# Performance work log

Hardware: AMD Instinct MI355X
Metric: run time of the kernel (lower is better)

## Reference

```python
import jax, jax.numpy as jnp
import numpy as np

N = 100000   # nodes
E = 500000   # edges
DN = 64      # node feat dim
DE = 64      # edge feat dim
D = 128      # hidden = in_feats = out_feats
TD = 64      # time-encoding dim


def setup_inputs() -> dict:
    key = jax.random.key(0)
    ks = jax.random.split(key, 20)
    s = 0.05
    inp = {
        'nfeat': jax.random.normal(ks[0], (N, DN), dtype=jnp.float32),
        'efeat': jax.random.normal(ks[1], (E, DE), dtype=jnp.float32),
        'src': jax.random.randint(ks[2], (E,), 0, N),
        'dst': jax.random.randint(ks[3], (E,), 0, N),
        'ts': jax.random.uniform(ks[4], (E,), dtype=jnp.float32) * 1000.0,
    }
    i = 5
    for l in (1, 2):
        inp[f'W_self{l}'] = jax.random.normal(ks[i], (D + TD, D), dtype=jnp.float32) * s; i += 1
        inp[f'b_self{l}'] = jnp.zeros((D,), dtype=jnp.float32)
        inp[f'W_neigh{l}'] = jax.random.normal(ks[i], (D, D), dtype=jnp.float32) * s; i += 1
        inp[f'b_neigh{l}'] = jnp.zeros((D,), dtype=jnp.float32)
        inp[f'omega{l}'] = jax.random.normal(ks[i], (TD,), dtype=jnp.float32); i += 1
        inp[f'phase{l}'] = jax.random.normal(ks[i], (TD,), dtype=jnp.float32); i += 1
    return inp


def _tsage_layer(src_prev, dst_prev, src, dst, ts, W_self, b_self, W_neigh, b_neigh, omega, phase):
    # cosine time encoding per edge: [E, TD]
    te = jnp.cos(ts[:, None] * omega[None, :] + phase[None, :])
    # temporal-neighborhood mean: per node, mean of features of incident edges
    sum_n = (jax.ops.segment_sum(dst_prev, src, num_segments=N)
             + jax.ops.segment_sum(src_prev, dst, num_segments=N))      # [N, D]
    ones = jnp.ones((src.shape[0], 1), dtype=src_prev.dtype)
    cnt = (jax.ops.segment_sum(ones, src, num_segments=N)
           + jax.ops.segment_sum(ones, dst, num_segments=N))            # [N, 1]
    mean_n = sum_n / jnp.maximum(cnt, 1.0)                              # [N, D]
    neigh_proj = mean_n @ W_neigh + b_neigh                             # project once per node
    src_out = jnp.concatenate([src_prev, te], axis=1) @ W_self + b_self + neigh_proj[src]
    dst_out = jnp.concatenate([dst_prev, te], axis=1) @ W_self + b_self + neigh_proj[dst]
    # dropout in eval mode (identity), then activation (relu)
    return jax.nn.relu(src_out), jax.nn.relu(dst_out)


def reference(nfeat, efeat, src, dst, ts,
              W_self1, b_self1, W_neigh1, b_neigh1, omega1, phase1,
              W_self2, b_self2, W_neigh2, b_neigh2, omega2, phase2):
    # combine_feats: per-edge gather-concat of endpoint node feats with edge feats
    src_feat = jnp.concatenate([nfeat[src], efeat], axis=1)  # [E, D]
    dst_feat = jnp.concatenate([nfeat[dst], efeat], axis=1)  # [E, D]
    params = [
        (W_self1, b_self1, W_neigh1, b_neigh1, omega1, phase1),
        (W_self2, b_self2, W_neigh2, b_neigh2, omega2, phase2),
    ]
    for p in params:
        src_feat, dst_feat = _tsage_layer(src_feat, dst_feat, src, dst, ts, *p)
    return src_feat, dst_feat
```

## Files before the change

kernel.cpp:

```cpp
#include <hip/hip_runtime.h>
#include <cstdint>
#include <cmath>

#define NN 100000
#define EE 500000
#define CAP 48

typedef __attribute__((ext_vector_type(8))) short short8v;
typedef __attribute__((ext_vector_type(4))) float f32x4;

static __device__ __forceinline__ unsigned short f2bf_rne(float x) {
    unsigned u = __float_as_uint(x);
    u += 0x7FFFu + ((u >> 16) & 1u);
    return (unsigned short)(u >> 16);
}

static __device__ __forceinline__ void split8(float4 a, float4 b,
                                              short8v* hi, short8v* lo) {
    union { short8v v; unsigned u[4]; } H, L;
    float f[8] = {a.x, a.y, a.z, a.w, b.x, b.y, b.z, b.w};
#pragma unroll
    for (int p = 0; p < 4; ++p) {
        unsigned u0 = __float_as_uint(f[2 * p]);
        unsigned u1 = __float_as_uint(f[2 * p + 1]);
        H.u[p] = (u0 >> 16) | (u1 & 0xFFFF0000u);
        float r0 = f[2 * p]     - __uint_as_float(u0 & 0xFFFF0000u);
        float r1 = f[2 * p + 1] - __uint_as_float(u1 & 0xFFFF0000u);
        L.u[p] = (unsigned)f2bf_rne(r0) | ((unsigned)f2bf_rne(r1) << 16);
    }
    *hi = H.v; *lo = L.v;
}

static __device__ __forceinline__ void lds_dma16(const void* g, void* l) {
    __builtin_amdgcn_global_load_lds(
        (const __attribute__((address_space(1))) unsigned int*)g,
        (__attribute__((address_space(3))) unsigned int*)l, 16, 0, 0);
}

__global__ __launch_bounds__(256) void k_build(const int* __restrict__ src,
                                               const int* __restrict__ dst,
                                               int* __restrict__ pos,
                                               int2* __restrict__ inc) {
    int e = blockIdx.x * 256 + threadIdx.x;
    if (e >= EE) return;
    int s = src[e], d = dst[e];
    int sl = atomicAdd(&pos[s], 1);
    if (sl < CAP) inc[(size_t)s * CAP + sl] = make_int2((e << 1) | 1, d);
    int dl = atomicAdd(&pos[d], 1);
    if (dl < CAP) inc[(size_t)d * CAP + dl] = make_int2((e << 1), s);
}

__global__ __launch_bounds__(256) void k_wt(const float* __restrict__ W, int K,
                                            unsigned short* __restrict__ H,
                                            unsigned short* __restrict__ L) {
    int idx = blockIdx.x * 256 + threadIdx.x;
    if (idx >= K * 128) return;
    int k = idx >> 7, c = idx & 127;
    float x = W[idx];
    unsigned u = __float_as_uint(x);
    H[(size_t)c * K + k] = (unsigned short)(u >> 16);
    float r = x - __uint_as_float(u & 0xFFFF0000u);
    L[(size_t)c * K + k] = f2bf_rne(r);
}

template <int LAYER>
__global__ __launch_bounds__(256) void k_agg(const float* __restrict__ featS,
                                             const float* __restrict__ featD,
                                             const float* __restrict__ nfeat,
                                             const float* __restrict__ efeat,
                                             const int* __restrict__ pos,
                                             const int2* __restrict__ inc,
                                             float* __restrict__ mean) {
    int w = (blockIdx.x * 256 + threadIdx.x) >> 6;
    int lane = threadIdx.x & 63;
    if (w >= NN) return;
    int q = lane >> 4, cl = lane & 15;
    int d = pos[w];
    int dd = min(d, CAP);
    const int2* lst = inc + (size_t)w * CAP;
    float a0 = 0.f, a1 = 0.f, a2 = 0.f, a3 = 0.f;
    float a4 = 0.f, a5 = 0.f, a6 = 0.f, a7 = 0.f;
    for (int j = q; j < dd; j += 4) {
        int2 en = lst[j];
        int e = en.x >> 1, side = en.x & 1;
        const float* p;
        if (LAYER == 1) {
            p = (cl < 8) ? (nfeat + (size_t)en.y * 64 + cl * 8)
                         : (efeat + (size_t)e * 64 + (cl - 8) * 8);
        } else {
            p = (side ? featD : featS) + (size_t)e * 128 + cl * 8;
        }
        float4 v0 = *(const float4*)p;
        float4 v1 = *(const float4*)(p + 4);
        a0 += v0.x; a1 += v0.y; a2 += v0.z; a3 += v0.w;
        a4 += v1.x; a5 += v1.y; a6 += v1.z; a7 += v1.w;
    }
#pragma unroll
    for (int m = 16; m <= 32; m <<= 1) {
        a0 += __shfl_xor(a0, m); a1 += __shfl_xor(a1, m);
        a2 += __shfl_xor(a2, m); a3 += __shfl_xor(a3, m);
        a4 += __shfl_xor(a4, m); a5 += __shfl_xor(a5, m);
        a6 += __shfl_xor(a6, m); a7 += __shfl_xor(a7, m);
    }
    if (q == 0) {
        float inv = 1.0f / fmaxf((float)d, 1.0f);
        float4 r0, r1;
        r0.x = a0 * inv; r0.y = a1 * inv; r0.z = a2 * inv; r0.w = a3 * inv;
        r1.x = a4 * inv; r1.y = a5 * inv; r1.z = a6 * inv; r1.w = a7 * inv;
        *(float4*)(mean + (size_t)w * 128 + cl * 8) = r0;
        *(float4*)(mean + (size_t)w * 128 + cl * 8 + 4) = r1;
    }
}

__global__ __launch_bounds__(256) void k_neigh_mfma(
        const float* __restrict__ mean,
        const unsigned short* __restrict__ WtH,
        const unsigned short* __restrict__ WtL,
        const float* __restrict__ bias,
        float* __restrict__ outp) {
    const int tid  = threadIdx.x;
    const int n0   = blockIdx.x * 128;
    const int lane = tid & 63;
    const int w    = tid >> 6;
    const int wr   = w >> 1, wc = w & 1;
    const int krow = lane & 15;
    const int kgrp = lane >> 4;

    const float* rb[4];
#pragma unroll
    for (int rt = 0; rt < 4; ++rt) {
        int n = min(n0 + wr * 64 + rt * 16 + krow, NN - 1);
        rb[rt] = mean + (size_t)n * 128;
    }

    f32x4 acc[4][4] = {};
#pragma unroll
    for (int ch = 0; ch < 4; ++ch) {
        const int koff = ch * 32 + kgrp * 8;
        short8v Ah[4], Al[4];
#pragma unroll
        for (int rt = 0; rt < 4; ++rt) {
            float4 x0 = *(const float4*)(rb[rt] + koff);
            float4 x1 = *(const float4*)(rb[rt] + koff + 4);
            split8(x0, x1, &Ah[rt], &Al[rt]);
        }
        short8v Bh[4], Bl[4];
#pragma unroll
        for (int ct = 0; ct < 4; ++ct) {
            int c = wc * 64 + ct * 16 + krow;
            Bh[ct] = *(const short8v*)(WtH + (size_t)c * 128 + koff);
            Bl[ct] = *(const short8v*)(WtL + (size_t)c * 128 + koff);
        }
#pragma unroll
        for (int ct = 0; ct < 4; ++ct)
#pragma unroll
            for (int rt = 0; rt < 4; ++rt) {
                acc[rt][ct] = __builtin_amdgcn_mfma_f32_16x16x32_bf16(Ah[rt], Bh[ct], acc[rt][ct], 0, 0, 0);
                acc[rt][ct] = __builtin_amdgcn_mfma_f32_16x16x32_bf16(Ah[rt], Bl[ct], acc[rt][ct], 0, 0, 0);
                acc[rt][ct] = __builtin_amdgcn_mfma_f32_16x16x32_bf16(Al[rt], Bh[ct], acc[rt][ct], 0, 0, 0);
            }
    }

    float bcol[4];
#pragma unroll
    for (int ct = 0; ct < 4; ++ct) bcol[ct] = bias[wc * 64 + ct * 16 + krow];
#pragma unroll
    for (int rt = 0; rt < 4; ++rt)
#pragma unroll
        for (int j = 0; j < 4; ++j) {
            int n = n0 + wr * 64 + rt * 16 + kgrp * 4 + j;
            if (n < NN) {
                float* op = outp + (size_t)n * 128;
#pragma unroll
                for (int ct = 0; ct < 4; ++ct)
                    op[wc * 64 + ct * 16 + krow] = acc[rt][ct][j] + bcol[ct];
            }
        }
}

template <int LAYER>
__global__ __launch_bounds__(256) void k_edge_mfma(
        const float* __restrict__ featS, const float* __restrict__ featD,
        const float* __restrict__ nfeat, const float* __restrict__ efeat,
        float* __restrict__ outS, float* __restrict__ outD,
        const int* __restrict__ src, const int* __restrict__ dst,
        const float* __restrict__ ts,
        const unsigned short* __restrict__ WtH,
        const unsigned short* __restrict__ WtL,
        const float* __restrict__ bias,
        const float* __restrict__ neigh,
        const float* __restrict__ omega, const float* __restrict__ phase) {
    __shared__ float Abuf[2][128][32];
    __shared__ unsigned short teH[64][72];
    __shared__ unsigned short teL[64][72];

    const int tid  = threadIdx.x;
    const int e0   = blockIdx.x * 64;
    const int lane = tid & 63;
    const int w    = tid >> 6;
    const int wr   = w >> 1, wc = w & 1;
    const int krow = lane & 15;
    const int kgrp = lane >> 4;

    {
        const int tl = tid & 63;
        const int j0 = (tid >> 6) * 16;
        const float tval = ts[min(e0 + tl, EE - 1)];
#pragma unroll
        for (int j = 0; j < 16; j += 2) {
            int jj = j0 + j;
            float c0 = cosf(fmaf(tval, omega[jj],     phase[jj]));
            float c1 = cosf(fmaf(tval, omega[jj + 1], phase[jj + 1]));
            unsigned u0 = __float_as_uint(c0), u1 = __float_as_uint(c1);
            *(unsigned*)&teH[tl][jj] = (u0 >> 16) | (u1 & 0xFFFF0000u);
            float r0 = c0 - __uint_as_float(u0 & 0xFFFF0000u);
            float r1 = c1 - __uint_as_float(u1 & 0xFFFF0000u);
            *(unsigned*)&teL[tl][jj] =
                (unsigned)f2bf_rne(r0) | ((unsigned)f2bf_rne(r1) << 16);
        }
    }

    const float* gbN[4];
    const float* gbE[4];
#pragma unroll
    for (int qq = 0; qq < 4; ++qq) {
        int row = w * 32 + qq * 8 + (lane >> 3);
        int e = min(e0 + (row & 63), EE - 1);
        if (LAYER == 1) {
            int node = (row < 64) ? src[e] : dst[e];
            gbN[qq] = nfeat + (size_t)node * 64;
            gbE[qq] = efeat + (size_t)e * 64;
        } else {
            gbN[qq] = ((row < 64) ? featS : featD) + (size_t)e * 128;
            gbE[qq] = nullptr;
        }
    }
    const int pslot = lane & 7;

    auto dma_chunk = [&](int b, int ch) {
#pragma unroll
        for (int qq = 0; qq < 4; ++qq) {
            int row = w * 32 + qq * 8 + (lane >> 3);
            int pg = (pslot - row) & 7;
            const float* gsrc;
            if (LAYER == 1)
                gsrc = ((ch < 2) ? (gbN[qq] + ch * 32) : (gbE[qq] + (ch - 2) * 32)) + pg * 4;
            else
                gsrc = gbN[qq] + ch * 32 + pg * 4;
            lds_dma16(gsrc, &Abuf[b][(w * 4 + qq) * 8][0]);
        }
    };

    f32x4 acc[4][4] = {};
    dma_chunk(0, 0);

#pragma unroll
    for (int ch = 0; ch < 4; ++ch) {
        __syncthreads();
        if (ch < 3) dma_chunk((ch + 1) & 1, ch + 1);
        const int b = ch & 1;
        const int koff = ch * 32 + kgrp * 8;
        short8v Ah[4], Al[4];
#pragma unroll
        for (int rt = 0; rt < 4; ++rt) {
            int row = wr * 64 + rt * 16 + krow;
            float4 x0 = *(const float4*)&Abuf[b][row][(((2 * kgrp)     + row) & 7) * 4];
            float4 x1 = *(const float4*)&Abuf[b][row][(((2 * kgrp + 1) + row) & 7) * 4];
            split8(x0, x1, &Ah[rt], &Al[rt]);
        }
        short8v Bh[4], Bl[4];
#pragma unroll
        for (int ct = 0; ct < 4; ++ct) {
            int c = wc * 64 + ct * 16 + krow;
            Bh[ct] = *(const short8v*)(WtH + (size_t)c * 192 + koff);
            Bl[ct] = *(const short8v*)(WtL + (size_t)c * 192 + koff);
        }
#pragma unroll
        for (int ct = 0; ct < 4; ++ct)
#pragma unroll
            for (int rt = 0; rt < 4; ++rt) {
                acc[rt][ct] = __builtin_amdgcn_mfma_f32_16x16x32_bf16(Ah[rt], Bh[ct], acc[rt][ct], 0, 0, 0);
                acc[rt][ct] = __builtin_amdgcn_mfma_f32_16x16x32_bf16(Ah[rt], Bl[ct], acc[rt][ct], 0, 0, 0);
                acc[rt][ct] = __builtin_amdgcn_mfma_f32_16x16x32_bf16(Al[rt], Bh[ct], acc[rt][ct], 0, 0, 0);
            }
    }

#pragma unroll
    for (int ch = 4; ch < 6; ++ch) {
        const int koff = ch * 32 + kgrp * 8;
        const int kt = koff - 128;
        short8v Ah[4], Al[4];
#pragma unroll
        for (int rt = 0; rt < 4; ++rt) {
            int el = rt * 16 + krow;
            Ah[rt] = *(const short8v*)&teH[el][kt];
            Al[rt] = *(const short8v*)&teL[el][kt];
        }
        short8v Bh[4], Bl[4];
#pragma unroll
        for (int ct = 0; ct < 4; ++ct) {
            int c = wc * 64 + ct * 16 + krow;
            Bh[ct] = *(const short8v*)(WtH + (size_t)c * 192 + koff);
            Bl[ct] = *(const short8v*)(WtL + (size_t)c * 192 + koff);
        }
#pragma unroll
        for (int ct = 0; ct < 4; ++ct)
#pragma unroll
            for (int rt = 0; rt < 4; ++rt) {
                acc[rt][ct] = __builtin_amdgcn_mfma_f32_16x16x32_bf16(Ah[rt], Bh[ct], acc[rt][ct], 0, 0, 0);
                acc[rt][ct] = __builtin_amdgcn_mfma_f32_16x16x32_bf16(Ah[rt], Bl[ct], acc[rt][ct], 0, 0, 0);
                acc[rt][ct] = __builtin_amdgcn_mfma_f32_16x16x32_bf16(Al[rt], Bh[ct], acc[rt][ct], 0, 0, 0);
            }
    }

    float bcol[4];
#pragma unroll
    for (int ct = 0; ct < 4; ++ct) bcol[ct] = bias[wc * 64 + ct * 16 + krow];
#pragma unroll
    for (int rt = 0; rt < 4; ++rt)
#pragma unroll
        for (int j = 0; j < 4; ++j) {
            int row = wr * 64 + rt * 16 + kgrp * 4 + j;
            int e = e0 + (row & 63);
            if (e < EE) {
                bool isS = row < 64;
                int node = isS ? src[e] : dst[e];
                const float* np = neigh + (size_t)node * 128;
                float* op = (isS ? outS : outD) + (size_t)e * 128;
#pragma unroll
                for (int ct = 0; ct < 4; ++ct) {
                    int col = wc * 64 + ct * 16 + krow;
                    float v2 = acc[rt][ct][j] + bcol[ct] + np[col];
                    op[col] = fmaxf(v2, 0.f);
                }
            }
        }
}

extern "C" void kernel_launch(void* const* d_in, const int* in_sizes, int n_in,
                              void* d_out, int out_size, void* d_ws, size_t ws_size,
                              hipStream_t stream) {
    const float* nfeat = (const float*)d_in[0];
    const float* efeat = (const float*)d_in[1];
    const int*   src   = (const int*)d_in[2];
    const int*   dst   = (const int*)d_in[3];
    const float* ts    = (const float*)d_in[4];
    const float* Wself[2]  = {(const float*)d_in[5],  (const float*)d_in[11]};
    const float* bself[2]  = {(const float*)d_in[6],  (const float*)d_in[12]};
    const float* Wneigh[2] = {(const float*)d_in[7],  (const float*)d_in[13]};
    const float* bneigh[2] = {(const float*)d_in[8],  (const float*)d_in[14]};
    const float* omega[2]  = {(const float*)d_in[9],  (const float*)d_in[15]};
    const float* phase[2]  = {(const float*)d_in[10], (const float*)d_in[16]};

    float* outS = (float*)d_out;
    float* outD = outS + (size_t)EE * 128;

    float* mean  = (float*)d_ws;
    float* neigh = mean + (size_t)NN * 128;
    int*   pos   = (int*)(neigh + (size_t)NN * 128);
    int2*  inc   = (int2*)(pos + NN);
    unsigned short* wb = (unsigned short*)(inc + (size_t)NN * CAP);
    unsigned short* WsH[2] = {wb,                 wb + 2 * 128 * 192};
    unsigned short* WsL[2] = {wb + 128 * 192,     wb + 3 * 128 * 192};
    unsigned short* wn = wb + 4 * 128 * 192;
    unsigned short* WnH[2] = {wn,                 wn + 2 * 128 * 128};
    unsigned short* WnL[2] = {wn + 128 * 128,     wn + 3 * 128 * 128};

    hipMemsetAsync(pos, 0, NN * sizeof(int), stream);
    k_build<<<(EE + 255) / 256, 256, 0, stream>>>(src, dst, pos, inc);
    for (int l = 0; l < 2; ++l) {
        k_wt<<<(192 * 128 + 255) / 256, 256, 0, stream>>>(Wself[l], 192, WsH[l], WsL[l]);
        k_wt<<<(128 * 128 + 255) / 256, 256, 0, stream>>>(Wneigh[l], 128, WnH[l], WnL[l]);
    }

    k_agg<1><<<(NN * 64 + 255) / 256, 256, 0, stream>>>(outS, outD, nfeat, efeat,
                                                        pos, inc, mean);
    k_neigh_mfma<<<(NN + 127) / 128, 256, 0, stream>>>(mean, WnH[0], WnL[0], bneigh[0], neigh);
    k_edge_mfma<1><<<(EE + 63) / 64, 256, 0, stream>>>(outS, outD, nfeat, efeat,
                                                       outS, outD, src, dst, ts,
                                                       WsH[0], WsL[0], bself[0], neigh,
                                                       omega[0], phase[0]);

    k_agg<2><<<(NN * 64 + 255) / 256, 256, 0, stream>>>(outS, outD, nfeat, efeat,
                                                        pos, inc, mean);
    k_neigh_mfma<<<(NN + 127) / 128, 256, 0, stream>>>(mean, WnH[1], WnL[1], bneigh[1], neigh);
    k_edge_mfma<2><<<(EE + 63) / 64, 256, 0, stream>>>(outS, outD, nfeat, efeat,
                                                       outS, outD, src, dst, ts,
                                                       WsH[1], WsL[1], bself[1], neigh,
                                                       omega[1], phase[1]);
}
```

Baseline: 1.913 ms.

## Fuse neighbor projection into edge GEMM by concatenating mean rows along K

Removes the separate per-node neighbor-projection kernel. Each edge row now gathers its endpoint's mean vector as four extra K-chunks and multiplies against a combined 320-row weight (W_self stacked with W_neigh), with both biases added in the epilogue. The A-tile staging moves from double to triple buffering with explicit vmcnt waits, and the aggregation loop prefetches the next incidence entry. This drops the neigh buffer round trip and its gather in the epilogue, but it redoes the 128x128 projection per edge endpoint (about 10x more MFMA work for that part) and gathers 512 B mean rows per edge row.

```diff
diff --git a/kernel.cpp b/kernel.cpp
--- a/kernel.cpp
+++ b/kernel.cpp
@@ -50,17 +50,18 @@
     if (dl < CAP) inc[(size_t)d * CAP + dl] = make_int2((e << 1), s);
 }
 
-__global__ __launch_bounds__(256) void k_wt(const float* __restrict__ W, int K,
-                                            unsigned short* __restrict__ H,
-                                            unsigned short* __restrict__ L) {
+__global__ __launch_bounds__(256) void k_wt2(const float* __restrict__ Wself,
+                                             const float* __restrict__ Wneigh,
+                                             unsigned short* __restrict__ H,
+                                             unsigned short* __restrict__ L) {
     int idx = blockIdx.x * 256 + threadIdx.x;
-    if (idx >= K * 128) return;
+    if (idx >= 320 * 128) return;
     int k = idx >> 7, c = idx & 127;
-    float x = W[idx];
+    float x = (k < 192) ? Wself[k * 128 + c] : Wneigh[(k - 192) * 128 + c];
     unsigned u = __float_as_uint(x);
-    H[(size_t)c * K + k] = (unsigned short)(u >> 16);
+    H[(size_t)c * 320 + k] = (unsigned short)(u >> 16);
     float r = x - __uint_as_float(u & 0xFFFF0000u);
-    L[(size_t)c * K + k] = f2bf_rne(r);
+    L[(size_t)c * 320 + k] = f2bf_rne(r);
 }
 
 template <int LAYER>
@@ -80,8 +81,9 @@
     const int2* lst = inc + (size_t)w * CAP;
     float a0 = 0.f, a1 = 0.f, a2 = 0.f, a3 = 0.f;
     float a4 = 0.f, a5 = 0.f, a6 = 0.f, a7 = 0.f;
+    int2 en = (q < dd) ? lst[q] : make_int2(0, 0);
     for (int j = q; j < dd; j += 4) {
-        int2 en = lst[j];
+        int2 nxt = (j + 4 < dd) ? lst[j + 4] : en;
         int e = en.x >> 1, side = en.x & 1;
         const float* p;
         if (LAYER == 1) {
@@ -94,6 +96,7 @@
         float4 v1 = *(const float4*)(p + 4);
         a0 += v0.x; a1 += v0.y; a2 += v0.z; a3 += v0.w;
         a4 += v1.x; a5 += v1.y; a6 += v1.z; a7 += v1.w;
+        en = nxt;
     }
 #pragma unroll
     for (int m = 16; m <= 32; m <<= 1) {
@@ -112,85 +115,19 @@
     }
 }
 
-__global__ __launch_bounds__(256) void k_neigh_mfma(
-        const float* __restrict__ mean,
-        const unsigned short* __restrict__ WtH,
-        const unsigned short* __restrict__ WtL,
-        const float* __restrict__ bias,
-        float* __restrict__ outp) {
-    const int tid  = threadIdx.x;
-    const int n0   = blockIdx.x * 128;
-    const int lane = tid & 63;
-    const int w    = tid >> 6;
-    const int wr   = w >> 1, wc = w & 1;
-    const int krow = lane & 15;
-    const int kgrp = lane >> 4;
-
-    const float* rb[4];
-#pragma unroll
-    for (int rt = 0; rt < 4; ++rt) {
-        int n = min(n0 + wr * 64 + rt * 16 + krow, NN - 1);
-        rb[rt] = mean + (size_t)n * 128;
-    }
-
-    f32x4 acc[4][4] = {};
-#pragma unroll
-    for (int ch = 0; ch < 4; ++ch) {
-        const int koff = ch * 32 + kgrp * 8;
-        short8v Ah[4], Al[4];
-#pragma unroll
-        for (int rt = 0; rt < 4; ++rt) {
-            float4 x0 = *(const float4*)(rb[rt] + koff);
-            float4 x1 = *(const float4*)(rb[rt] + koff + 4);
-            split8(x0, x1, &Ah[rt], &Al[rt]);
-        }
-        short8v Bh[4], Bl[4];
-#pragma unroll
-        for (int ct = 0; ct < 4; ++ct) {
-            int c = wc * 64 + ct * 16 + krow;
-            Bh[ct] = *(const short8v*)(WtH + (size_t)c * 128 + koff);
-            Bl[ct] = *(const short8v*)(WtL + (size_t)c * 128 + koff);
-        }
-#pragma unroll
-        for (int ct = 0; ct < 4; ++ct)
-#pragma unroll
-            for (int rt = 0; rt < 4; ++rt) {
-                acc[rt][ct] = __builtin_amdgcn_mfma_f32_16x16x32_bf16(Ah[rt], Bh[ct], acc[rt][ct], 0, 0, 0);
-                acc[rt][ct] = __builtin_amdgcn_mfma_f32_16x16x32_bf16(Ah[rt], Bl[ct], acc[rt][ct], 0, 0, 0);
-                acc[rt][ct] = __builtin_amdgcn_mfma_f32_16x16x32_bf16(Al[rt], Bh[ct], acc[rt][ct], 0, 0, 0);
-            }
-    }
-
-    float bcol[4];
-#pragma unroll
-    for (int ct = 0; ct < 4; ++ct) bcol[ct] = bias[wc * 64 + ct * 16 + krow];
-#pragma unroll
-    for (int rt = 0; rt < 4; ++rt)
-#pragma unroll
-        for (int j = 0; j < 4; ++j) {
-            int n = n0 + wr * 64 + rt * 16 + kgrp * 4 + j;
-            if (n < NN) {
-                float* op = outp + (size_t)n * 128;
-#pragma unroll
-                for (int ct = 0; ct < 4; ++ct)
-                    op[wc * 64 + ct * 16 + krow] = acc[rt][ct][j] + bcol[ct];
-            }
-        }
-}
-
 template <int LAYER>
-__global__ __launch_bounds__(256) void k_edge_mfma(
+__global__ __launch_bounds__(256) void k_edge_fused(
         const float* __restrict__ featS, const float* __restrict__ featD,
         const float* __restrict__ nfeat, const float* __restrict__ efeat,
+        const float* __restrict__ mean,
         float* __restrict__ outS, float* __restrict__ outD,
         const int* __restrict__ src, const int* __restrict__ dst,
         const float* __restrict__ ts,
         const unsigned short* __restrict__ WtH,
         const unsigned short* __restrict__ WtL,
-        const float* __restrict__ bias,
-        const float* __restrict__ neigh,
+        const float* __restrict__ bs, const float* __restrict__ bn,
         const float* __restrict__ omega, const float* __restrict__ phase) {
-    __shared__ float Abuf[2][128][32];
+    __shared__ float Abuf[3][128][32];
     __shared__ unsigned short teH[64][72];
     __shared__ unsigned short teL[64][72];
 
@@ -219,48 +156,77 @@
                 (unsigned)f2bf_rne(r0) | ((unsigned)f2bf_rne(r1) << 16);
         }
     }
-
-    const float* gbN[4];
+    asm volatile("s_waitcnt lgkmcnt(0)" ::: "memory");
+    __builtin_amdgcn_sched_barrier(0);
+
+    int nodeq[4];
+    const float* gbF[4];
     const float* gbE[4];
 #pragma unroll
     for (int qq = 0; qq < 4; ++qq) {
         int row = w * 32 + qq * 8 + (lane >> 3);
         int e = min(e0 + (row & 63), EE - 1);
+        int node = (row < 64) ? src[e] : dst[e];
+        nodeq[qq] = node;
         if (LAYER == 1) {
-            int node = (row < 64) ? src[e] : dst[e];
-            gbN[qq] = nfeat + (size_t)node * 64;
+            gbF[qq] = nfeat + (size_t)node * 64;
             gbE[qq] = efeat + (size_t)e * 64;
         } else {
-            gbN[qq] = ((row < 64) ? featS : featD) + (size_t)e * 128;
+            gbF[qq] = ((row < 64) ? featS : featD) + (size_t)e * 128;
             gbE[qq] = nullptr;
         }
     }
     const int pslot = lane & 7;
 
-    auto dma_chunk = [&](int b, int ch) {
+    auto dma = [&](int j) {
 #pragma unroll
         for (int qq = 0; qq < 4; ++qq) {
             int row = w * 32 + qq * 8 + (lane >> 3);
             int pg = (pslot - row) & 7;
             const float* gsrc;
-            if (LAYER == 1)
-                gsrc = ((ch < 2) ? (gbN[qq] + ch * 32) : (gbE[qq] + (ch - 2) * 32)) + pg * 4;
-            else
-                gsrc = gbN[qq] + ch * 32 + pg * 4;
-            lds_dma16(gsrc, &Abuf[b][(w * 4 + qq) * 8][0]);
+            if (j < 4) {
+                if (LAYER == 1)
+                    gsrc = (j < 2) ? (gbF[qq] + j * 32 + pg * 4)
+                                   : (gbE[qq] + (j - 2) * 32 + pg * 4);
+                else
+                    gsrc = gbF[qq] + j * 32 + pg * 4;
+            } else {
+                gsrc = mean + (size_t)nodeq[qq] * 128 + (j - 4) * 32 + pg * 4;
+            }
+            lds_dma16(gsrc, &Abuf[j % 3][(w * 4 + qq) * 8][0]);
         }
     };
 
     f32x4 acc[4][4] = {};
-    dma_chunk(0, 0);
-
-#pragma unroll
-    for (int ch = 0; ch < 4; ++ch) {
-        __syncthreads();
-        if (ch < 3) dma_chunk((ch + 1) & 1, ch + 1);
-        const int b = ch & 1;
-        const int koff = ch * 32 + kgrp * 8;
+
+    dma(0);
+    dma(1);
+    asm volatile("s_waitcnt vmcnt(4)" ::: "memory");
+    __builtin_amdgcn_sched_barrier(0);
+
+#pragma unroll
+    for (int j = 0; j < 8; ++j) {
+        const int kb = (j < 4) ? j * 32 : 192 + (j - 4) * 32;
+        __builtin_amdgcn_s_barrier();
+        __builtin_amdgcn_sched_barrier(0);
+
+        const int koff = kb + kgrp * 8;
+        short8v Bh[4], Bl[4];
+#pragma unroll
+        for (int ct = 0; ct < 4; ++ct) {
+            int c = wc * 64 + ct * 16 + krow;
+            Bh[ct] = *(const short8v*)(WtH + (size_t)c * 320 + koff);
+            Bl[ct] = *(const short8v*)(WtL + (size_t)c * 320 + koff);
+        }
+        __builtin_amdgcn_sched_barrier(0);
+        if (j < 6) dma(j + 2);
+        __builtin_amdgcn_sched_barrier(0);
+        if (j < 7) { asm volatile("s_waitcnt vmcnt(4)" ::: "memory"); }
+        else       { asm volatile("s_waitcnt vmcnt(0)" ::: "memory"); }
+        __builtin_amdgcn_sched_barrier(0);
+
         short8v Ah[4], Al[4];
+        const int b = j % 3;
 #pragma unroll
         for (int rt = 0; rt < 4; ++rt) {
             int row = wr * 64 + rt * 16 + krow;
@@ -268,13 +234,6 @@
             float4 x1 = *(const float4*)&Abuf[b][row][(((2 * kgrp + 1) + row) & 7) * 4];
             split8(x0, x1, &Ah[rt], &Al[rt]);
         }
-        short8v Bh[4], Bl[4];
-#pragma unroll
-        for (int ct = 0; ct < 4; ++ct) {
-            int c = wc * 64 + ct * 16 + krow;
-            Bh[ct] = *(const short8v*)(WtH + (size_t)c * 192 + koff);
-            Bl[ct] = *(const short8v*)(WtL + (size_t)c * 192 + koff);
-        }
 #pragma unroll
         for (int ct = 0; ct < 4; ++ct)
 #pragma unroll
@@ -286,22 +245,23 @@
     }
 
 #pragma unroll
-    for (int ch = 4; ch < 6; ++ch) {
-        const int koff = ch * 32 + kgrp * 8;
-        const int kt = koff - 128;
+    for (int tc = 0; tc < 2; ++tc) {
+        const int kb = 128 + tc * 32;
+        const int koff = kb + kgrp * 8;
+        const int kt = tc * 32 + kgrp * 8;
+        short8v Bh[4], Bl[4];
+#pragma unroll
+        for (int ct = 0; ct < 4; ++ct) {
+            int c = wc * 64 + ct * 16 + krow;
+            Bh[ct] = *(const short8v*)(WtH + (size_t)c * 320 + koff);
+            Bl[ct] = *(const short8v*)(WtL + (size_t)c * 320 + koff);
+        }
         short8v Ah[4], Al[4];
 #pragma unroll
         for (int rt = 0; rt < 4; ++rt) {
             int el = rt * 16 + krow;
             Ah[rt] = *(const short8v*)&teH[el][kt];
             Al[rt] = *(const short8v*)&teL[el][kt];
-        }
-        short8v Bh[4], Bl[4];
-#pragma unroll
-        for (int ct = 0; ct < 4; ++ct) {
-            int c = wc * 64 + ct * 16 + krow;
-            Bh[ct] = *(const short8v*)(WtH + (size_t)c * 192 + koff);
-            Bl[ct] = *(const short8v*)(WtL + (size_t)c * 192 + koff);
         }
 #pragma unroll
         for (int ct = 0; ct < 4; ++ct)
@@ -315,23 +275,22 @@
 
     float bcol[4];
 #pragma unroll
-    for (int ct = 0; ct < 4; ++ct) bcol[ct] = bias[wc * 64 + ct * 16 + krow];
+    for (int ct = 0; ct < 4; ++ct) {
+        int col = wc * 64 + ct * 16 + krow;
+        bcol[ct] = bs[col] + bn[col];
+    }
 #pragma unroll
     for (int rt = 0; rt < 4; ++rt)
 #pragma unroll
-        for (int j = 0; j < 4; ++j) {
-            int row = wr * 64 + rt * 16 + kgrp * 4 + j;
+        for (int jj = 0; jj < 4; ++jj) {
+            int row = wr * 64 + rt * 16 + kgrp * 4 + jj;
             int e = e0 + (row & 63);
             if (e < EE) {
-                bool isS = row < 64;
-                int node = isS ? src[e] : dst[e];
-                const float* np = neigh + (size_t)node * 128;
-                float* op = (isS ? outS : outD) + (size_t)e * 128;
+                float* op = ((row < 64) ? outS : outD) + (size_t)e * 128;
 #pragma unroll
                 for (int ct = 0; ct < 4; ++ct) {
                     int col = wc * 64 + ct * 16 + krow;
-                    float v2 = acc[rt][ct][j] + bcol[ct] + np[col];
-                    op[col] = fmaxf(v2, 0.f);
+                    op[col] = fmaxf(acc[rt][ct][jj] + bcol[ct], 0.f);
                 }
             }
         }
@@ -355,37 +314,29 @@
     float* outS = (float*)d_out;
     float* outD = outS + (size_t)EE * 128;
 
-    float* mean  = (float*)d_ws;
-    float* neigh = mean + (size_t)NN * 128;
-    int*   pos   = (int*)(neigh + (size_t)NN * 128);
-    int2*  inc   = (int2*)(pos + NN);
+    float* mean = (float*)d_ws;
+    int*   pos  = (int*)(mean + (size_t)NN * 128);
+    int2*  inc  = (int2*)(pos + NN);
     unsigned short* wb = (unsigned short*)(inc + (size_t)NN * CAP);
-    unsigned short* WsH[2] = {wb,                 wb + 2 * 128 * 192};
-    unsigned short* WsL[2] = {wb + 128 * 192,     wb + 3 * 128 * 192};
-    unsigned short* wn = wb + 4 * 128 * 192;
-    unsigned short* WnH[2] = {wn,                 wn + 2 * 128 * 128};
-    unsigned short* WnL[2] = {wn + 128 * 128,     wn + 3 * 128 * 128};
+    unsigned short* WH[2] = {wb,                 wb + 2 * 320 * 128};
+    unsigned short* WL[2] = {wb + 320 * 128,     wb + 3 * 320 * 128};
 
     hipMemsetAsync(pos, 0, NN * sizeof(int), stream);
     k_build<<<(EE + 255) / 256, 256, 0, stream>>>(src, dst, pos, inc);
-    for (int l = 0; l < 2; ++l) {
-        k_wt<<<(192 * 128 + 255) / 256, 256, 0, stream>>>(Wself[l], 192, WsH[l], WsL[l]);
-        k_wt<<<(128 * 128 + 255) / 256, 256, 0, stream>>>(Wneigh[l], 128, WnH[l], WnL[l]);
-    }
+    for (int l = 0; l < 2; ++l)
+        k_wt2<<<(320 * 128 + 255) / 256, 256, 0, stream>>>(Wself[l], Wneigh[l], WH[l], WL[l]);
 
     k_agg<1><<<(NN * 64 + 255) / 256, 256, 0, stream>>>(outS, outD, nfeat, efeat,
                                                         pos, inc, mean);
-    k_neigh_mfma<<<(NN + 127) / 128, 256, 0, stream>>>(mean, WnH[0], WnL[0], bneigh[0], neigh);
-    k_edge_mfma<1><<<(EE + 63) / 64, 256, 0, stream>>>(outS, outD, nfeat, efeat,
-                                                       outS, outD, src, dst, ts,
-                                                       WsH[0], WsL[0], bself[0], neigh,
-                                                       omega[0], phase[0]);
+    k_edge_fused<1><<<(EE + 63) / 64, 256, 0, stream>>>(outS, outD, nfeat, efeat, mean,
+                                                        outS, outD, src, dst, ts,
+                                                        WH[0], WL[0], bself[0], bneigh[0],
+                                                        omega[0], phase[0]);
 
     k_agg<2><<<(NN * 64 + 255) / 256, 256, 0, stream>>>(outS, outD, nfeat, efeat,
                                                         pos, inc, mean);
-    k_neigh_mfma<<<(NN + 127) / 128, 256, 0, stream>>>(mean, WnH[1], WnL[1], bneigh[1], neigh);
-    k_edge_mfma<2><<<(EE + 63) / 64, 256, 0, stream>>>(outS, outD, nfeat, efeat,
-                                                       outS, outD, src, dst, ts,
-                                                       WsH[1], WsL[1], bself[1], neigh,
-                                                       omega[1], phase[1]);
-}
+    k_edge_fused<2><<<(EE + 63) / 64, 256, 0, stream>>>(outS, outD, nfeat, efeat, mean,
+                                                        outS, outD, src, dst, ts,
+                                                        WH[1], WL[1], bself[1], bneigh[1],
+                                                        omega[1], phase[1]);
+}
```

After: 1.854 ms. 3.1% less time.
